# Kernel optimization log

Hardware: AMD Instinct MI355X
Metric: run time of the kernel (lower is better)

Reference implementation:

```python
import jax, jax.numpy as jnp
import numpy as np

B, S, D, H = 2, 2048, 1024, 16
DK = D // H

def setup_inputs() -> dict:
    key = jax.random.key(0)
    ks = jax.random.split(key, 9)
    def lin(k, fan_in):
        bound = 1.0 / np.sqrt(fan_in)
        kw, kb = jax.random.split(k)
        w = jax.random.uniform(kw, (D, D), jnp.float32, -bound, bound)
        b = jax.random.uniform(kb, (D,), jnp.float32, -bound, bound)
        return w, b
    Wq_w, Wq_b = lin(ks[0], D)
    Wk_w, Wk_b = lin(ks[1], D)
    Wv_w, Wv_b = lin(ks[2], D)
    Wo_w, Wo_b = lin(ks[3], D)
    x = jax.random.normal(ks[4], (B, S, D), jnp.float32)
    mask = jnp.ones((B, 1, 1, S), jnp.int32)
    return {"x": x, "mask": mask,
            "Wq_w": Wq_w, "Wq_b": Wq_b, "Wk_w": Wk_w, "Wk_b": Wk_b,
            "Wv_w": Wv_w, "Wv_b": Wv_b, "Wo_w": Wo_w, "Wo_b": Wo_b}

def reference(x, mask, Wq_w, Wq_b, Wk_w, Wk_b, Wv_w, Wv_b, Wo_w, Wo_b):
    b, s, d = x.shape
    def split_heads(t):  # [B,S,D] -> [B,H,S,DK]
        return t.reshape(b, s, H, DK).transpose(0, 2, 1, 3)
    Q = split_heads(x @ Wq_w.T + Wq_b)
    K = split_heads(x @ Wk_w.T + Wk_b)
    V = split_heads(x @ Wv_w.T + Wv_b)
    scale = 1.0 / jnp.sqrt(jnp.float32(DK))
    scores = jnp.einsum('bhqd,bhkd->bhqk', Q, K) * scale  # [B,H,S,S]
    scores = jnp.where(mask == 0, jnp.float32(-1e9), scores)
    attn = jax.nn.softmax(scores, axis=-1)
    context = jnp.einsum('bhqk,bhkd->bhqd', attn, V)  # [B,H,S,DK]
    context = context.transpose(0, 2, 1, 3).reshape(b, s, d)
    return context @ Wo_w.T + Wo_b
```

## Files before the change

kernel.cpp:

```cpp
#include <hip/hip_runtime.h>
#include <hip/hip_bf16.h>


#define DEV __device__ __forceinline__

typedef __bf16 bf16_t;
typedef __bf16 bf16x4 __attribute__((ext_vector_type(4)));
typedef __bf16 bf16x8 __attribute__((ext_vector_type(8)));
typedef float f32x4 __attribute__((ext_vector_type(4)));

constexpr int Ss = 2048, Dd = 1024, Hh = 16, DKk = 64;

DEV void gload_lds16(const void* g, void* l) {
  __builtin_amdgcn_global_load_lds(
      (__attribute__((address_space(1))) void*)(g),
      (__attribute__((address_space(3))) void*)(l), 16, 0, 0);
}

DEV bf16_t f2b(float v) { return (bf16_t)v; }

DEV void cvt16_core(const float* src, bf16_t* dst) {
  const float4* s4 = (const float4*)src;
  float4 a = s4[0], b = s4[1], c = s4[2], d = s4[3];
  bf16x8 lo = {f2b(a.x), f2b(a.y), f2b(a.z), f2b(a.w), f2b(b.x), f2b(b.y), f2b(b.z), f2b(b.w)};
  bf16x8 hi = {f2b(c.x), f2b(c.y), f2b(c.z), f2b(c.w), f2b(d.x), f2b(d.y), f2b(d.z), f2b(d.w)};
  *(bf16x8*)dst = lo;
  *(bf16x8*)(dst + 8) = hi;
}

__global__ __launch_bounds__(256) void cvt16(const float* __restrict__ x,
                                             bf16_t* __restrict__ xb) {
  size_t i = ((size_t)blockIdx.x * 256 + threadIdx.x) * 16;
  cvt16_core(x + i, xb + i);
}

__global__ __launch_bounds__(256) void cvt_all(
    const float* __restrict__ x,
    const float* __restrict__ wq, const float* __restrict__ wk,
    const float* __restrict__ wv, const float* __restrict__ wo,
    bf16_t* __restrict__ xb, bf16_t* __restrict__ Wb) {
  size_t i = ((size_t)blockIdx.x * 256 + threadIdx.x) * 16;
  const size_t XN = (size_t)4 << 20;
  if (i < XN) {
    cvt16_core(x + i, xb + i);
  } else {
    size_t j = i - XN;
    int z = (int)(j >> 20);
    size_t o = j & (((size_t)1 << 20) - 1);
    const float* s = (z == 0) ? wq : ((z == 1) ? wk : ((z == 2) ? wv : wo));
    cvt16_core(s + o, Wb + j);
  }
}

template <bool WB16>
__global__ __launch_bounds__(256) void gemm_qkv(
    const bf16_t* __restrict__ A,
    const float* __restrict__ W0, const float* __restrict__ W1, const float* __restrict__ W2,
    const bf16_t* __restrict__ Wb,
    const float* __restrict__ b0, const float* __restrict__ b1, const float* __restrict__ b2,
    bf16_t* __restrict__ o0, bf16_t* __restrict__ o1, bf16_t* __restrict__ o2) {
  const int z = blockIdx.z;
  const float* Wf = (z == 0) ? W0 : ((z == 1) ? W1 : W2);
  const bf16_t* Wbf = Wb + (size_t)z * (1u << 20);
  const float* bias = (z == 0) ? b0 : ((z == 1) ? b1 : b2);
  bf16_t* out = (z == 0) ? o0 : ((z == 1) ? o1 : o2);

  __shared__ __align__(16) bf16_t As[128 * 32];
  __shared__ __align__(16) bf16_t Ws[128 * 32];

  const int tid = threadIdx.x;
  const int lane = tid & 63, w = tid >> 6;
  const int quad = lane >> 4, c = lane & 15;
  const int wm = w >> 1, wn = w & 1;
  const int m0 = blockIdx.y * 128, n0 = blockIdx.x * 128;
  const int trow = tid >> 1, tcol = (tid & 1) * 16;
  const int srow = lane >> 2, scol = (lane & 3) * 8;

  const f32x4 vzero = {0.f, 0.f, 0.f, 0.f};
  f32x4 acc[4][4];
  for (int i = 0; i < 4; i++)
    for (int j = 0; j < 4; j++) acc[i][j] = vzero;

  for (int k0 = 0; k0 < 1024; k0 += 32) {
    for (int r = 0; r < 2; r++) {
      int row = r * 64 + w * 16;
      gload_lds16(&A[(size_t)(m0 + row + srow) * 1024 + k0 + scol], &As[row * 32]);
      if (WB16)
        gload_lds16(&Wbf[(size_t)(n0 + row + srow) * 1024 + k0 + scol], &Ws[row * 32]);
    }
    if (!WB16)
      cvt16_core(&Wf[(size_t)(n0 + trow) * 1024 + k0 + tcol], &Ws[trow * 32 + tcol]);
    __syncthreads();

    bf16x8 af[4], bfr[4];
    for (int i = 0; i < 4; i++)
      af[i] = *(const bf16x8*)&As[(wm * 64 + i * 16 + c) * 32 + quad * 8];
    for (int j = 0; j < 4; j++)
      bfr[j] = *(const bf16x8*)&Ws[(wn * 64 + j * 16 + c) * 32 + quad * 8];
    for (int i = 0; i < 4; i++)
      for (int j = 0; j < 4; j++)
        acc[i][j] = __builtin_amdgcn_mfma_f32_16x16x32_bf16(af[i], bfr[j], acc[i][j], 0, 0, 0);
    __syncthreads();
  }

  for (int j = 0; j < 4; j++) {
    int n = n0 + wn * 64 + j * 16 + c;
    float bv = bias[n];
    for (int i = 0; i < 4; i++) {
      int mbase = m0 + wm * 64 + i * 16 + quad * 4;
      int b_ = mbase >> 11, s_ = mbase & 2047;
      int h_ = n >> 6, dk_ = n & 63;
      if (z < 2) {
        for (int r = 0; r < 4; r++)
          out[((size_t)(b_ * Hh + h_) * Ss + (s_ + r)) * DKk + dk_] =
              f2b(acc[i][j][r] + bv);
      } else {
        bf16x4 pk;
        for (int r = 0; r < 4; r++) pk[r] = f2b(acc[i][j][r] + bv);
        *(bf16x4*)&out[((size_t)(b_ * Hh + h_) * DKk + dk_) * Ss + s_] = pk;
      }
    }
  }
}

__global__ __launch_bounds__(256) void attn_fwd(
    const bf16_t* __restrict__ Q, const bf16_t* __restrict__ K,
    const bf16_t* __restrict__ Vt, const int* __restrict__ mask,
    bf16_t* __restrict__ ctx) {
  __shared__ __align__(16) bf16_t Ks[2][64 * 64];
  __shared__ __align__(16) bf16_t Vts[2][64 * 64];
  __shared__ __align__(16) bf16_t Ps[4][32 * 64];

  const int tid = threadIdx.x, lane = tid & 63, w = tid >> 6;
  const int quad = lane >> 4, c = lane & 15;
  const int c7 = c & 7;
  const int bh = blockIdx.y, b_ = bh >> 4, h_ = bh & 15;
  const int q0 = blockIdx.x * 128 + w * 32;
  const size_t head = (size_t)bh * Ss * DKk;
  const int* maskb = mask + b_ * Ss;

  const int sr = lane >> 3;
  const int gc = (lane & 7) ^ sr;

  {
    for (int r = 0; r < 2; r++) {
      int row = r * 32 + w * 8;
      gload_lds16(&K[head + (size_t)(row + sr) * 64 + gc * 8], &Ks[0][row * 64]);
      gload_lds16(&Vt[head + (size_t)(row + sr) * Ss + gc * 8], &Vts[0][row * 64]);
    }
  }

  bf16x8 qf[2][2];
  for (int mi = 0; mi < 2; mi++)
    for (int ks = 0; ks < 2; ks++)
      qf[mi][ks] = *(const bf16x8*)&Q[head + (size_t)(q0 + mi * 16 + c) * DKk + ks * 32 + quad * 8];

  int mk[4];
  for (int ni = 0; ni < 4; ni++) mk[ni] = maskb[ni * 16 + c];

  const bf16_t oneb = f2b(1.0f);
  const bf16x8 ones = {oneb, oneb, oneb, oneb, oneb, oneb, oneb, oneb};

  const f32x4 vzero = {0.f, 0.f, 0.f, 0.f};
  f32x4 o[2][4];
  for (int mi = 0; mi < 2; mi++)
    for (int j = 0; j < 4; j++) o[mi][j] = vzero;
  f32x4 ol[2] = {vzero, vzero};

  constexpr int NT = Ss / 64;
  for (int kt = 0; kt < NT; kt++) {
    const int cur = kt & 1;
    __syncthreads();

    if (kt + 1 < NT) {
      int nxt = cur ^ 1;
      for (int r = 0; r < 2; r++) {
        int row = r * 32 + w * 8;
        gload_lds16(&K[head + (size_t)((kt + 1) * 64 + row + sr) * 64 + gc * 8],
                    &Ks[nxt][row * 64]);
        gload_lds16(&Vt[head + (size_t)(row + sr) * Ss + (kt + 1) * 64 + gc * 8],
                    &Vts[nxt][row * 64]);
      }
    }
    int mkn[4];
    if (kt + 1 < NT)
      for (int ni = 0; ni < 4; ni++) mkn[ni] = maskb[(kt + 1) * 64 + ni * 16 + c];

    f32x4 sc[2][4];
    for (int mi = 0; mi < 2; mi++)
      for (int ni = 0; ni < 4; ni++) sc[mi][ni] = vzero;
    for (int ks = 0; ks < 2; ks++) {
      int pc = ((ks * 4 + quad) ^ c7) * 8;
      for (int ni = 0; ni < 4; ni++) {
        bf16x8 kf = *(const bf16x8*)&Ks[cur][(ni * 16 + c) * 64 + pc];
        sc[0][ni] = __builtin_amdgcn_mfma_f32_16x16x32_bf16(qf[0][ks], kf, sc[0][ni], 0, 0, 0);
        sc[1][ni] = __builtin_amdgcn_mfma_f32_16x16x32_bf16(qf[1][ks], kf, sc[1][ni], 0, 0, 0);
      }
    }

    for (int ni = 0; ni < 4; ni++) {
      for (int mi = 0; mi < 2; mi++)
        for (int r = 0; r < 4; r++) {
          float p = __expf(sc[mi][ni][r] * 0.125f);
          sc[mi][ni][r] = mk[ni] ? p : 0.f;
        }
    }

    for (int mi = 0; mi < 2; mi++)
      for (int ni = 0; ni < 4; ni++)
        for (int r = 0; r < 4; r++) {
          int ql = mi * 16 + quad * 4 + r;
          int chunk = (ni * 2 + (c >> 3)) ^ (ql & 7);
          Ps[w][ql * 64 + chunk * 8 + c7] = f2b(sc[mi][ni][r]);
        }

    for (int ks = 0; ks < 2; ks++) {
      int pc = ((ks * 4 + quad) ^ c7) * 8;
      bf16x8 pf0 = *(const bf16x8*)&Ps[w][(c)*64 + pc];
      bf16x8 pf1 = *(const bf16x8*)&Ps[w][(16 + c) * 64 + pc];
      for (int j = 0; j < 4; j++) {
        bf16x8 vf = *(const bf16x8*)&Vts[cur][(j * 16 + c) * 64 + pc];
        o[0][j] = __builtin_amdgcn_mfma_f32_16x16x32_bf16(pf0, vf, o[0][j], 0, 0, 0);
        o[1][j] = __builtin_amdgcn_mfma_f32_16x16x32_bf16(pf1, vf, o[1][j], 0, 0, 0);
      }
      ol[0] = __builtin_amdgcn_mfma_f32_16x16x32_bf16(pf0, ones, ol[0], 0, 0, 0);
      ol[1] = __builtin_amdgcn_mfma_f32_16x16x32_bf16(pf1, ones, ol[1], 0, 0, 0);
    }

    for (int ni = 0; ni < 4; ni++) mk[ni] = mkn[ni];
  }

  for (int mi = 0; mi < 2; mi++) {
    float inv[4];
    for (int r = 0; r < 4; r++) inv[r] = 1.0f / ol[mi][r];
    for (int j = 0; j < 4; j++)
      for (int r = 0; r < 4; r++) {
        int s_ = q0 + mi * 16 + quad * 4 + r;
        ctx[((size_t)(b_ * Ss + s_)) * Dd + h_ * 64 + j * 16 + c] =
            f2b(o[mi][j][r] * inv[r]);
      }
  }
}

template <bool WB16>
__global__ __launch_bounds__(256) void gemm_out(
    const bf16_t* __restrict__ A, const float* __restrict__ Wf,
    const bf16_t* __restrict__ Wb, const float* __restrict__ bias,
    float* __restrict__ out) {
  __shared__ __align__(16) bf16_t As[64 * 32];
  __shared__ __align__(16) bf16_t Ws[128 * 32];

  const int tid = threadIdx.x;
  const int lane = tid & 63, w = tid >> 6;
  const int quad = lane >> 4, c = lane & 15;
  const int wm = w >> 1, wn = w & 1;
  const int m0 = blockIdx.y * 64, n0 = blockIdx.x * 128;
  const int trow = tid >> 1, tcol = (tid & 1) * 16;
  const int srow = lane >> 2, scol = (lane & 3) * 8;

  const f32x4 vzero = {0.f, 0.f, 0.f, 0.f};
  f32x4 acc[2][4];
  for (int i = 0; i < 2; i++)
    for (int j = 0; j < 4; j++) acc[i][j] = vzero;

  for (int k0 = 0; k0 < 1024; k0 += 32) {
    gload_lds16(&A[(size_t)(m0 + w * 16 + srow) * 1024 + k0 + scol], &As[(w * 16) * 32]);
    if (WB16) {
      for (int r = 0; r < 2; r++) {
        int row = r * 64 + w * 16;
        gload_lds16(&Wb[(size_t)(n0 + row + srow) * 1024 + k0 + scol], &Ws[row * 32]);
      }
    } else {
      cvt16_core(&Wf[(size_t)(n0 + trow) * 1024 + k0 + tcol], &Ws[trow * 32 + tcol]);
    }
    __syncthreads();

    bf16x8 af[2], bfr[4];
    for (int i = 0; i < 2; i++)
      af[i] = *(const bf16x8*)&As[(wm * 32 + i * 16 + c) * 32 + quad * 8];
    for (int j = 0; j < 4; j++)
      bfr[j] = *(const bf16x8*)&Ws[(wn * 64 + j * 16 + c) * 32 + quad * 8];
    for (int i = 0; i < 2; i++)
      for (int j = 0; j < 4; j++)
        acc[i][j] = __builtin_amdgcn_mfma_f32_16x16x32_bf16(af[i], bfr[j], acc[i][j], 0, 0, 0);
    __syncthreads();
  }

  for (int j = 0; j < 4; j++) {
    int n = n0 + wn * 64 + j * 16 + c;
    float bv = bias[n];
    for (int i = 0; i < 2; i++) {
      int mbase = m0 + wm * 32 + i * 16 + quad * 4;
      for (int r = 0; r < 4; r++)
        out[(size_t)(mbase + r) * 1024 + n] = acc[i][j][r] + bv;
    }
  }
}

extern "C" void kernel_launch(void* const* d_in, const int* in_sizes, int n_in,
                              void* d_out, int out_size, void* d_ws, size_t ws_size,
                              hipStream_t stream) {
  const float* x  = (const float*)d_in[0];
  const int* mask = (const int*)d_in[1];
  const float* Wq = (const float*)d_in[2];
  const float* bq = (const float*)d_in[3];
  const float* Wk = (const float*)d_in[4];
  const float* bk = (const float*)d_in[5];
  const float* Wv = (const float*)d_in[6];
  const float* bv = (const float*)d_in[7];
  const float* Wo = (const float*)d_in[8];
  const float* bo = (const float*)d_in[9];
  float* out = (float*)d_out;

  bf16_t* ws = (bf16_t*)d_ws;
  const size_t QKV_ELEMS = (size_t)2 * Hh * Ss * DKk;
  bf16_t* xb  = ws;
  bf16_t* Qb  = ws + QKV_ELEMS;
  bf16_t* Kb  = ws + 2 * QKV_ELEMS;
  bf16_t* Vt  = ws + 3 * QKV_ELEMS;
  bf16_t* Wb  = ws + 4 * QKV_ELEMS;
  bf16_t* ctx = xb;

  const bool wb16 = ws_size >= (size_t)40 * 1024 * 1024;

  if (wb16) {
    cvt_all<<<dim3(2048), 256, 0, stream>>>(x, Wq, Wk, Wv, Wo, xb, Wb);
    gemm_qkv<true><<<dim3(8, 32, 3), 256, 0, stream>>>(
        xb, Wq, Wk, Wv, Wb, bq, bk, bv, Qb, Kb, Vt);
  } else {
    cvt16<<<dim3(1024), 256, 0, stream>>>(x, xb);
    gemm_qkv<false><<<dim3(8, 32, 3), 256, 0, stream>>>(
        xb, Wq, Wk, Wv, ws , bq, bk, bv, Qb, Kb, Vt);
  }
  attn_fwd<<<dim3(Ss / 128, 2 * Hh), 256, 0, stream>>>(Qb, Kb, Vt, mask, ctx);
  if (wb16)
    gemm_out<true><<<dim3(8, 64), 256, 0, stream>>>(ctx, Wo, Wb + 3 * (1u << 20), bo, out);
  else
    gemm_out<false><<<dim3(8, 64), 256, 0, stream>>>(ctx, Wo, ws , bo, out);
}
```

Before: 220.1 us.

## Keep softmax probabilities in registers via transposed QK MFMA, fold scale into Q

Computes S^T = K·Q^T so each lane's score fragment maps directly onto an MFMA A-operand, feeding P to the PV MFMA from registers with half-zero-padded operands instead of round-tripping through LDS. The softmax scale and log2(e) are folded into the Q projection epilogue so the kernel uses raw exp2, and the mask becomes an additive bias loaded as int4. Attention blocks shrink to 128 threads covering 64 queries, which doubles the grid. The cost is that half of each PV MFMA is zero padding, so the PV matrix work doubles, in exchange for removing the LDS write/read and their bank traffic.

```diff
diff --git a/kernel.cpp b/kernel.cpp
--- a/kernel.cpp
+++ b/kernel.cpp
@@ -10,6 +10,7 @@
 typedef float f32x4 __attribute__((ext_vector_type(4)));
 
 constexpr int Ss = 2048, Dd = 1024, Hh = 16, DKk = 64;
+constexpr float QSCALE = 0.125f * 1.4426950408889634f;
 
 DEV void gload_lds16(const void* g, void* l) {
   __builtin_amdgcn_global_load_lds(
@@ -18,6 +19,14 @@
 }
 
 DEV bf16_t f2b(float v) { return (bf16_t)v; }
+
+DEV float fast_exp2(float x) {
+#if __has_builtin(__builtin_amdgcn_exp2f)
+  return __builtin_amdgcn_exp2f(x);
+#else
+  return exp2f(x);
+#endif
+}
 
 DEV void cvt16_core(const float* src, bf16_t* dst) {
   const float4* s4 = (const float4*)src;
@@ -64,6 +73,7 @@
   const bf16_t* Wbf = Wb + (size_t)z * (1u << 20);
   const float* bias = (z == 0) ? b0 : ((z == 1) ? b1 : b2);
   bf16_t* out = (z == 0) ? o0 : ((z == 1) ? o1 : o2);
+  const float oscale = (z == 0) ? QSCALE : 1.0f;
 
   __shared__ __align__(16) bf16_t As[128 * 32];
   __shared__ __align__(16) bf16_t Ws[128 * 32];
@@ -113,7 +123,7 @@
       if (z < 2) {
         for (int r = 0; r < 4; r++)
           out[((size_t)(b_ * Hh + h_) * Ss + (s_ + r)) * DKk + dk_] =
-              f2b(acc[i][j][r] + bv);
+              f2b((acc[i][j][r] + bv) * oscale);
       } else {
         bf16x4 pk;
         for (int r = 0; r < 4; r++) pk[r] = f2b(acc[i][j][r] + bv);
@@ -123,31 +133,28 @@
   }
 }
 
-__global__ __launch_bounds__(256) void attn_fwd(
+__global__ __launch_bounds__(128) void attn_fwd(
     const bf16_t* __restrict__ Q, const bf16_t* __restrict__ K,
     const bf16_t* __restrict__ Vt, const int* __restrict__ mask,
     bf16_t* __restrict__ ctx) {
   __shared__ __align__(16) bf16_t Ks[2][64 * 64];
   __shared__ __align__(16) bf16_t Vts[2][64 * 64];
-  __shared__ __align__(16) bf16_t Ps[4][32 * 64];
 
   const int tid = threadIdx.x, lane = tid & 63, w = tid >> 6;
   const int quad = lane >> 4, c = lane & 15;
   const int c7 = c & 7;
   const int bh = blockIdx.y, b_ = bh >> 4, h_ = bh & 15;
-  const int q0 = blockIdx.x * 128 + w * 32;
+  const int q0 = blockIdx.x * 64 + w * 32;
   const size_t head = (size_t)bh * Ss * DKk;
   const int* maskb = mask + b_ * Ss;
 
   const int sr = lane >> 3;
   const int gc = (lane & 7) ^ sr;
 
-  {
-    for (int r = 0; r < 2; r++) {
-      int row = r * 32 + w * 8;
-      gload_lds16(&K[head + (size_t)(row + sr) * 64 + gc * 8], &Ks[0][row * 64]);
-      gload_lds16(&Vt[head + (size_t)(row + sr) * Ss + gc * 8], &Vts[0][row * 64]);
-    }
+  for (int r = 0; r < 4; r++) {
+    int row = w * 32 + r * 8;
+    gload_lds16(&K[head + (size_t)(row + sr) * 64 + gc * 8], &Ks[0][row * 64]);
+    gload_lds16(&Vt[head + (size_t)(row + sr) * Ss + gc * 8], &Vts[0][row * 64]);
   }
 
   bf16x8 qf[2][2];
@@ -155,16 +162,16 @@
     for (int ks = 0; ks < 2; ks++)
       qf[mi][ks] = *(const bf16x8*)&Q[head + (size_t)(q0 + mi * 16 + c) * DKk + ks * 32 + quad * 8];
 
-  int mk[4];
-  for (int ni = 0; ni < 4; ni++) mk[ni] = maskb[ni * 16 + c];
-
-  const bf16_t oneb = f2b(1.0f);
-  const bf16x8 ones = {oneb, oneb, oneb, oneb, oneb, oneb, oneb, oneb};
+  int4 mk4[4];
+  for (int ni = 0; ni < 4; ni++) mk4[ni] = *(const int4*)&maskb[ni * 16 + quad * 4];
+
+  const bf16_t oneb = f2b(1.0f), zb = f2b(0.0f);
+  const bf16x8 ones = {oneb, oneb, oneb, oneb, zb, zb, zb, zb};
 
   const f32x4 vzero = {0.f, 0.f, 0.f, 0.f};
   f32x4 o[2][4];
   for (int mi = 0; mi < 2; mi++)
-    for (int j = 0; j < 4; j++) o[mi][j] = vzero;
+    for (int t = 0; t < 4; t++) o[mi][t] = vzero;
   f32x4 ol[2] = {vzero, vzero};
 
   constexpr int NT = Ss / 64;
@@ -174,17 +181,18 @@
 
     if (kt + 1 < NT) {
       int nxt = cur ^ 1;
-      for (int r = 0; r < 2; r++) {
-        int row = r * 32 + w * 8;
+      for (int r = 0; r < 4; r++) {
+        int row = w * 32 + r * 8;
         gload_lds16(&K[head + (size_t)((kt + 1) * 64 + row + sr) * 64 + gc * 8],
                     &Ks[nxt][row * 64]);
         gload_lds16(&Vt[head + (size_t)(row + sr) * Ss + (kt + 1) * 64 + gc * 8],
                     &Vts[nxt][row * 64]);
       }
     }
-    int mkn[4];
+    int4 mk4n[4];
     if (kt + 1 < NT)
-      for (int ni = 0; ni < 4; ni++) mkn[ni] = maskb[(kt + 1) * 64 + ni * 16 + c];
+      for (int ni = 0; ni < 4; ni++)
+        mk4n[ni] = *(const int4*)&maskb[(kt + 1) * 64 + ni * 16 + quad * 4];
 
     f32x4 sc[2][4];
     for (int mi = 0; mi < 2; mi++)
@@ -193,51 +201,49 @@
       int pc = ((ks * 4 + quad) ^ c7) * 8;
       for (int ni = 0; ni < 4; ni++) {
         bf16x8 kf = *(const bf16x8*)&Ks[cur][(ni * 16 + c) * 64 + pc];
-        sc[0][ni] = __builtin_amdgcn_mfma_f32_16x16x32_bf16(qf[0][ks], kf, sc[0][ni], 0, 0, 0);
-        sc[1][ni] = __builtin_amdgcn_mfma_f32_16x16x32_bf16(qf[1][ks], kf, sc[1][ni], 0, 0, 0);
-      }
-    }
-
+        sc[0][ni] = __builtin_amdgcn_mfma_f32_16x16x32_bf16(kf, qf[0][ks], sc[0][ni], 0, 0, 0);
+        sc[1][ni] = __builtin_amdgcn_mfma_f32_16x16x32_bf16(kf, qf[1][ks], sc[1][ni], 0, 0, 0);
+      }
+    }
+
+    f32x4 mb[4];
     for (int ni = 0; ni < 4; ni++) {
-      for (int mi = 0; mi < 2; mi++)
-        for (int r = 0; r < 4; r++) {
-          float p = __expf(sc[mi][ni][r] * 0.125f);
-          sc[mi][ni][r] = mk[ni] ? p : 0.f;
-        }
-    }
-
-    for (int mi = 0; mi < 2; mi++)
-      for (int ni = 0; ni < 4; ni++)
-        for (int r = 0; r < 4; r++) {
-          int ql = mi * 16 + quad * 4 + r;
-          int chunk = (ni * 2 + (c >> 3)) ^ (ql & 7);
-          Ps[w][ql * 64 + chunk * 8 + c7] = f2b(sc[mi][ni][r]);
-        }
-
-    for (int ks = 0; ks < 2; ks++) {
-      int pc = ((ks * 4 + quad) ^ c7) * 8;
-      bf16x8 pf0 = *(const bf16x8*)&Ps[w][(c)*64 + pc];
-      bf16x8 pf1 = *(const bf16x8*)&Ps[w][(16 + c) * 64 + pc];
-      for (int j = 0; j < 4; j++) {
-        bf16x8 vf = *(const bf16x8*)&Vts[cur][(j * 16 + c) * 64 + pc];
-        o[0][j] = __builtin_amdgcn_mfma_f32_16x16x32_bf16(pf0, vf, o[0][j], 0, 0, 0);
-        o[1][j] = __builtin_amdgcn_mfma_f32_16x16x32_bf16(pf1, vf, o[1][j], 0, 0, 0);
-      }
-      ol[0] = __builtin_amdgcn_mfma_f32_16x16x32_bf16(pf0, ones, ol[0], 0, 0, 0);
-      ol[1] = __builtin_amdgcn_mfma_f32_16x16x32_bf16(pf1, ones, ol[1], 0, 0, 0);
-    }
-
-    for (int ni = 0; ni < 4; ni++) mk[ni] = mkn[ni];
+      mb[ni][0] = mk4[ni].x ? 0.f : -1e9f;
+      mb[ni][1] = mk4[ni].y ? 0.f : -1e9f;
+      mb[ni][2] = mk4[ni].z ? 0.f : -1e9f;
+      mb[ni][3] = mk4[ni].w ? 0.f : -1e9f;
+    }
+
+    for (int ni = 0; ni < 4; ni++) {
+      bf16x8 a0, a1;
+      for (int r = 0; r < 4; r++) {
+        a0[r] = f2b(fast_exp2(sc[0][ni][r] + mb[ni][r]));
+        a1[r] = f2b(fast_exp2(sc[1][ni][r] + mb[ni][r]));
+        a0[4 + r] = zb;
+        a1[4 + r] = zb;
+      }
+      const int vcol = (((ni * 2 + (quad >> 1)) ^ c7) * 8) + (quad & 1) * 4;
+      for (int t = 0; t < 4; t++) {
+        bf16x4 v4 = *(const bf16x4*)&Vts[cur][(t * 16 + c) * 64 + vcol];
+        bf16x8 vf = {v4[0], v4[1], v4[2], v4[3], zb, zb, zb, zb};
+        o[0][t] = __builtin_amdgcn_mfma_f32_16x16x32_bf16(a0, vf, o[0][t], 0, 0, 0);
+        o[1][t] = __builtin_amdgcn_mfma_f32_16x16x32_bf16(a1, vf, o[1][t], 0, 0, 0);
+      }
+      ol[0] = __builtin_amdgcn_mfma_f32_16x16x32_bf16(a0, ones, ol[0], 0, 0, 0);
+      ol[1] = __builtin_amdgcn_mfma_f32_16x16x32_bf16(a1, ones, ol[1], 0, 0, 0);
+    }
+
+    for (int ni = 0; ni < 4; ni++) mk4[ni] = mk4n[ni];
   }
 
   for (int mi = 0; mi < 2; mi++) {
     float inv[4];
     for (int r = 0; r < 4; r++) inv[r] = 1.0f / ol[mi][r];
-    for (int j = 0; j < 4; j++)
+    for (int t = 0; t < 4; t++)
       for (int r = 0; r < 4; r++) {
         int s_ = q0 + mi * 16 + quad * 4 + r;
-        ctx[((size_t)(b_ * Ss + s_)) * Dd + h_ * 64 + j * 16 + c] =
-            f2b(o[mi][j][r] * inv[r]);
+        ctx[((size_t)(b_ * Ss + s_)) * Dd + h_ * 64 + t * 16 + c] =
+            f2b(o[mi][t][r] * inv[r]);
       }
   }
 }
@@ -332,7 +338,7 @@
     gemm_qkv<false><<<dim3(8, 32, 3), 256, 0, stream>>>(
         xb, Wq, Wk, Wv, ws , bq, bk, bv, Qb, Kb, Vt);
   }
-  attn_fwd<<<dim3(Ss / 128, 2 * Hh), 256, 0, stream>>>(Qb, Kb, Vt, mask, ctx);
+  attn_fwd<<<dim3(Ss / 64, 2 * Hh), 128, 0, stream>>>(Qb, Kb, Vt, mask, ctx);
   if (wb16)
     gemm_out<true><<<dim3(8, 64), 256, 0, stream>>>(ctx, Wo, Wb + 3 * (1u << 20), bo, out);
   else
```

Measured after the change: 222.2 us. Within noise of the previous version (+0.9%).

## Halve attention query tile per wave and fold softmax scale into Q projection

Applied to the files above, without the earlier changes.

The attention kernel now gives each wave 16 query rows instead of 32, so each block covers 64 queries and the grid doubles to 1024 blocks. This raises parallelism and cuts registers per wave, but every K/V tile is now loaded from global memory twice as often overall. The softmax scale and log2(e) are folded into Q in the projection epilogue, so the inner loop uses a bare exp2 plus an additive mask bias instead of a multiply, exp and select. The base kernel already skipped the max-subtraction in softmax; this version keeps that, and the extra exp2 scaling does not change its overflow risk.

```diff
diff --git a/kernel.cpp b/kernel.cpp
--- a/kernel.cpp
+++ b/kernel.cpp
@@ -10,6 +10,7 @@
 typedef float f32x4 __attribute__((ext_vector_type(4)));
 
 constexpr int Ss = 2048, Dd = 1024, Hh = 16, DKk = 64;
+constexpr float QSCALE = 0.125f * 1.4426950408889634f;
 
 DEV void gload_lds16(const void* g, void* l) {
   __builtin_amdgcn_global_load_lds(
@@ -18,6 +19,14 @@
 }
 
 DEV bf16_t f2b(float v) { return (bf16_t)v; }
+
+DEV float fast_exp2(float x) {
+#if __has_builtin(__builtin_amdgcn_exp2f)
+  return __builtin_amdgcn_exp2f(x);
+#else
+  return exp2f(x);
+#endif
+}
 
 DEV void cvt16_core(const float* src, bf16_t* dst) {
   const float4* s4 = (const float4*)src;
@@ -64,6 +73,7 @@
   const bf16_t* Wbf = Wb + (size_t)z * (1u << 20);
   const float* bias = (z == 0) ? b0 : ((z == 1) ? b1 : b2);
   bf16_t* out = (z == 0) ? o0 : ((z == 1) ? o1 : o2);
+  const float oscale = (z == 0) ? QSCALE : 1.0f;
 
   __shared__ __align__(16) bf16_t As[128 * 32];
   __shared__ __align__(16) bf16_t Ws[128 * 32];
@@ -113,7 +123,7 @@
       if (z < 2) {
         for (int r = 0; r < 4; r++)
           out[((size_t)(b_ * Hh + h_) * Ss + (s_ + r)) * DKk + dk_] =
-              f2b(acc[i][j][r] + bv);
+              f2b((acc[i][j][r] + bv) * oscale);
       } else {
         bf16x4 pk;
         for (int r = 0; r < 4; r++) pk[r] = f2b(acc[i][j][r] + bv);
@@ -129,31 +139,28 @@
     bf16_t* __restrict__ ctx) {
   __shared__ __align__(16) bf16_t Ks[2][64 * 64];
   __shared__ __align__(16) bf16_t Vts[2][64 * 64];
-  __shared__ __align__(16) bf16_t Ps[4][32 * 64];
+  __shared__ __align__(16) bf16_t Ps[4][16 * 64];
 
   const int tid = threadIdx.x, lane = tid & 63, w = tid >> 6;
   const int quad = lane >> 4, c = lane & 15;
   const int c7 = c & 7;
   const int bh = blockIdx.y, b_ = bh >> 4, h_ = bh & 15;
-  const int q0 = blockIdx.x * 128 + w * 32;
+  const int q0 = blockIdx.x * 64 + w * 16;
   const size_t head = (size_t)bh * Ss * DKk;
   const int* maskb = mask + b_ * Ss;
 
   const int sr = lane >> 3;
   const int gc = (lane & 7) ^ sr;
 
-  {
-    for (int r = 0; r < 2; r++) {
-      int row = r * 32 + w * 8;
-      gload_lds16(&K[head + (size_t)(row + sr) * 64 + gc * 8], &Ks[0][row * 64]);
-      gload_lds16(&Vt[head + (size_t)(row + sr) * Ss + gc * 8], &Vts[0][row * 64]);
-    }
-  }
-
-  bf16x8 qf[2][2];
-  for (int mi = 0; mi < 2; mi++)
-    for (int ks = 0; ks < 2; ks++)
-      qf[mi][ks] = *(const bf16x8*)&Q[head + (size_t)(q0 + mi * 16 + c) * DKk + ks * 32 + quad * 8];
+  for (int r = 0; r < 2; r++) {
+    int row = w * 16 + r * 8;
+    gload_lds16(&K[head + (size_t)(row + sr) * 64 + gc * 8], &Ks[0][row * 64]);
+    gload_lds16(&Vt[head + (size_t)(row + sr) * Ss + gc * 8], &Vts[0][row * 64]);
+  }
+
+  bf16x8 qf[2];
+  for (int ks = 0; ks < 2; ks++)
+    qf[ks] = *(const bf16x8*)&Q[head + (size_t)(q0 + c) * DKk + ks * 32 + quad * 8];
 
   int mk[4];
   for (int ni = 0; ni < 4; ni++) mk[ni] = maskb[ni * 16 + c];
@@ -162,10 +169,9 @@
   const bf16x8 ones = {oneb, oneb, oneb, oneb, oneb, oneb, oneb, oneb};
 
   const f32x4 vzero = {0.f, 0.f, 0.f, 0.f};
-  f32x4 o[2][4];
-  for (int mi = 0; mi < 2; mi++)
-    for (int j = 0; j < 4; j++) o[mi][j] = vzero;
-  f32x4 ol[2] = {vzero, vzero};
+  f32x4 o[4];
+  for (int t = 0; t < 4; t++) o[t] = vzero;
+  f32x4 ol = vzero;
 
   constexpr int NT = Ss / 64;
   for (int kt = 0; kt < NT; kt++) {
@@ -175,7 +181,7 @@
     if (kt + 1 < NT) {
       int nxt = cur ^ 1;
       for (int r = 0; r < 2; r++) {
-        int row = r * 32 + w * 8;
+        int row = w * 16 + r * 8;
         gload_lds16(&K[head + (size_t)((kt + 1) * 64 + row + sr) * 64 + gc * 8],
                     &Ks[nxt][row * 64]);
         gload_lds16(&Vt[head + (size_t)(row + sr) * Ss + (kt + 1) * 64 + gc * 8],
@@ -186,60 +192,47 @@
     if (kt + 1 < NT)
       for (int ni = 0; ni < 4; ni++) mkn[ni] = maskb[(kt + 1) * 64 + ni * 16 + c];
 
-    f32x4 sc[2][4];
-    for (int mi = 0; mi < 2; mi++)
-      for (int ni = 0; ni < 4; ni++) sc[mi][ni] = vzero;
+    f32x4 sc[4];
+    for (int ni = 0; ni < 4; ni++) sc[ni] = vzero;
     for (int ks = 0; ks < 2; ks++) {
       int pc = ((ks * 4 + quad) ^ c7) * 8;
       for (int ni = 0; ni < 4; ni++) {
         bf16x8 kf = *(const bf16x8*)&Ks[cur][(ni * 16 + c) * 64 + pc];
-        sc[0][ni] = __builtin_amdgcn_mfma_f32_16x16x32_bf16(qf[0][ks], kf, sc[0][ni], 0, 0, 0);
-        sc[1][ni] = __builtin_amdgcn_mfma_f32_16x16x32_bf16(qf[1][ks], kf, sc[1][ni], 0, 0, 0);
+        sc[ni] = __builtin_amdgcn_mfma_f32_16x16x32_bf16(qf[ks], kf, sc[ni], 0, 0, 0);
       }
     }
 
     for (int ni = 0; ni < 4; ni++) {
-      for (int mi = 0; mi < 2; mi++)
-        for (int r = 0; r < 4; r++) {
-          float p = __expf(sc[mi][ni][r] * 0.125f);
-          sc[mi][ni][r] = mk[ni] ? p : 0.f;
-        }
-    }
-
-    for (int mi = 0; mi < 2; mi++)
-      for (int ni = 0; ni < 4; ni++)
-        for (int r = 0; r < 4; r++) {
-          int ql = mi * 16 + quad * 4 + r;
-          int chunk = (ni * 2 + (c >> 3)) ^ (ql & 7);
-          Ps[w][ql * 64 + chunk * 8 + c7] = f2b(sc[mi][ni][r]);
-        }
+      float mb = mk[ni] ? 0.f : -1e9f;
+      for (int r = 0; r < 4; r++) {
+        float p = fast_exp2(sc[ni][r] + mb);
+        int ql = quad * 4 + r;
+        int chunk = (ni * 2 + (c >> 3)) ^ (ql & 7);
+        Ps[w][ql * 64 + chunk * 8 + c7] = f2b(p);
+      }
+    }
 
     for (int ks = 0; ks < 2; ks++) {
       int pc = ((ks * 4 + quad) ^ c7) * 8;
-      bf16x8 pf0 = *(const bf16x8*)&Ps[w][(c)*64 + pc];
-      bf16x8 pf1 = *(const bf16x8*)&Ps[w][(16 + c) * 64 + pc];
-      for (int j = 0; j < 4; j++) {
-        bf16x8 vf = *(const bf16x8*)&Vts[cur][(j * 16 + c) * 64 + pc];
-        o[0][j] = __builtin_amdgcn_mfma_f32_16x16x32_bf16(pf0, vf, o[0][j], 0, 0, 0);
-        o[1][j] = __builtin_amdgcn_mfma_f32_16x16x32_bf16(pf1, vf, o[1][j], 0, 0, 0);
-      }
-      ol[0] = __builtin_amdgcn_mfma_f32_16x16x32_bf16(pf0, ones, ol[0], 0, 0, 0);
-      ol[1] = __builtin_amdgcn_mfma_f32_16x16x32_bf16(pf1, ones, ol[1], 0, 0, 0);
+      bf16x8 pf = *(const bf16x8*)&Ps[w][c * 64 + pc];
+      for (int t = 0; t < 4; t++) {
+        bf16x8 vf = *(const bf16x8*)&Vts[cur][(t * 16 + c) * 64 + pc];
+        o[t] = __builtin_amdgcn_mfma_f32_16x16x32_bf16(pf, vf, o[t], 0, 0, 0);
+      }
+      ol = __builtin_amdgcn_mfma_f32_16x16x32_bf16(pf, ones, ol, 0, 0, 0);
     }
 
     for (int ni = 0; ni < 4; ni++) mk[ni] = mkn[ni];
   }
 
-  for (int mi = 0; mi < 2; mi++) {
-    float inv[4];
-    for (int r = 0; r < 4; r++) inv[r] = 1.0f / ol[mi][r];
-    for (int j = 0; j < 4; j++)
-      for (int r = 0; r < 4; r++) {
-        int s_ = q0 + mi * 16 + quad * 4 + r;
-        ctx[((size_t)(b_ * Ss + s_)) * Dd + h_ * 64 + j * 16 + c] =
-            f2b(o[mi][j][r] * inv[r]);
-      }
-  }
+  float inv[4];
+  for (int r = 0; r < 4; r++) inv[r] = 1.0f / ol[r];
+  for (int t = 0; t < 4; t++)
+    for (int r = 0; r < 4; r++) {
+      int s_ = q0 + quad * 4 + r;
+      ctx[((size_t)(b_ * Ss + s_)) * Dd + h_ * 64 + t * 16 + c] =
+          f2b(o[t][r] * inv[r]);
+    }
 }
 
 template <bool WB16>
@@ -332,7 +325,7 @@
     gemm_qkv<false><<<dim3(8, 32, 3), 256, 0, stream>>>(
         xb, Wq, Wk, Wv, ws , bq, bk, bv, Qb, Kb, Vt);
   }
-  attn_fwd<<<dim3(Ss / 128, 2 * Hh), 256, 0, stream>>>(Qb, Kb, Vt, mask, ctx);
+  attn_fwd<<<dim3(Ss / 64, 2 * Hh), 256, 0, stream>>>(Qb, Kb, Vt, mask, ctx);
   if (wb16)
     gemm_out<true><<<dim3(8, 64), 256, 0, stream>>>(ctx, Wo, Wb + 3 * (1u << 20), bo, out);
   else
```

New measurement: 230.0 us. 1.04x slower.
